# Optimization experiments

Measured on AMD Instinct MI355X. Metric: run time of the kernel, lower is better.

Reference implementation:

```python
import jax, jax.numpy as jnp
import numpy as np

S, V, E, H = 4096, 10000, 128, 256
NE, TK, NH, HD, FF, NL = 4, 2, 4, 64, 2048, 2
EPS = 1e-5
SCALE = 1.0 / np.sqrt(HD).astype(np.float32)


def setup_inputs() -> dict:
    key = jax.random.key(0)
    ks = iter(jax.random.split(key, 64))
    n = lambda shape: jax.random.normal(next(ks), shape, jnp.float32) * 0.02
    inp = {"x": jax.random.randint(next(ks), (S,), 0, V)}
    inp["emb"] = n((V, E))
    for i, din in enumerate([E, H, H]):
        inp[f"moe{i}_gw"] = n((NE, din))
        inp[f"moe{i}_gb"] = jnp.zeros((NE,), jnp.float32)
        inp[f"moe{i}_ew"] = n((NE, H, din))
        inp[f"moe{i}_eb"] = jnp.zeros((NE, H), jnp.float32)
    inp["attn_in_w"] = n((NL, 3 * H, H)); inp["attn_in_b"] = jnp.zeros((NL, 3 * H), jnp.float32)
    inp["attn_out_w"] = n((NL, H, H));    inp["attn_out_b"] = jnp.zeros((NL, H), jnp.float32)
    inp["ln1_g"] = jnp.ones((NL, H), jnp.float32); inp["ln1_b"] = jnp.zeros((NL, H), jnp.float32)
    inp["ln2_g"] = jnp.ones((NL, H), jnp.float32); inp["ln2_b"] = jnp.zeros((NL, H), jnp.float32)
    inp["ff1_w"] = n((NL, FF, H)); inp["ff1_b"] = jnp.zeros((NL, FF), jnp.float32)
    inp["ff2_w"] = n((NL, H, FF)); inp["ff2_b"] = jnp.zeros((NL, H), jnp.float32)
    inp["fc_w"] = n((H, H)); inp["fc_b"] = jnp.zeros((H,), jnp.float32)
    inp["out_w"] = n((V, H)); inp["out_b"] = jnp.zeros((V,), jnp.float32)
    return inp


def _ln(x, g, b):
    m = x.mean(-1, keepdims=True)
    v = ((x - m) ** 2).mean(-1, keepdims=True)
    return (x - m) * jax.lax.rsqrt(v + EPS) * g + b


def _moe(x, gw, gb, ew, eb):
    # x: [S, din]. Faithful quirk: experts are the top-k of TOKEN 0's gates,
    # applied to every token, weighted by each token's own top-k gate scores.
    scores = jax.nn.softmax(x @ gw.T + gb, axis=-1)            # [S, NE]
    vals, idx = jax.lax.top_k(scores, TK)                      # [S, TK]
    sel = idx[0]                                               # [TK]
    outs = jnp.einsum('si,khi->skh', x, ew[sel]) + eb[sel][None]  # [S, TK, H]
    return (outs * vals[:, :, None]).sum(axis=1)               # [S, H]


def reference(x, emb,
              moe0_gw, moe0_gb, moe0_ew, moe0_eb,
              moe1_gw, moe1_gb, moe1_ew, moe1_eb,
              moe2_gw, moe2_gb, moe2_ew, moe2_eb,
              attn_in_w, attn_in_b, attn_out_w, attn_out_b,
              ln1_g, ln1_b, ln2_g, ln2_b,
              ff1_w, ff1_b, ff2_w, ff2_b,
              fc_w, fc_b, out_w, out_b):
    h = emb[x]                                                 # [S, E]
    for gw, gb, ew, eb in [(moe0_gw, moe0_gb, moe0_ew, moe0_eb),
                           (moe1_gw, moe1_gb, moe1_ew, moe1_eb),
                           (moe2_gw, moe2_gb, moe2_ew, moe2_eb)]:
        h = _moe(h, gw, gb, ew, eb)                            # [S, H]
    for l in range(NL):  # post-norm TransformerEncoderLayer (relu, no dropout at eval)
        qkv = h @ attn_in_w[l].T + attn_in_b[l]                # [S, 3H]
        q, k, v = [t.reshape(S, NH, HD) for t in jnp.split(qkv, 3, axis=-1)]
        att = jax.nn.softmax(jnp.einsum('shd,thd->hst', q, k) * SCALE, axis=-1)
        a = jnp.einsum('hst,thd->shd', att, v).reshape(S, H)
        h = _ln(h + a @ attn_out_w[l].T + attn_out_b[l], ln1_g[l], ln1_b[l])
        ffh = jax.nn.relu(h @ ff1_w[l].T + ff1_b[l]) @ ff2_w[l].T + ff2_b[l]
        h = _ln(h + ffh, ln2_g[l], ln2_b[l])
    h = h @ fc_w.T + fc_b                                      # [S, H]
    logits = h @ out_w.T + out_b                               # [S, V]
    return jax.nn.log_softmax(logits, axis=-1)
```

## Files before the change

kernel.cpp:

```cpp
#include <hip/hip_runtime.h>
#include <math.h>

#define S_ 4096
#define V_ 10000
#define E_ 128
#define H_ 256
#define NE_ 4
#define NH_ 4
#define HD_ 64
#define FF_ 2048
#define NL_ 2
#define EPS_ 1e-5f
#define SCALE_ 0.125f
#define SPLITS_ 4

typedef __attribute__((ext_vector_type(8))) short bf16x8;
typedef __attribute__((ext_vector_type(4))) float f32x4;

static __device__ __forceinline__ short f2bf(float f) {
  unsigned u = __builtin_bit_cast(unsigned, f);
  unsigned r = (u + 0x7fffu + ((u >> 16) & 1u)) >> 16;
  return (short)r;
}
static __device__ __forceinline__ float bf2f(short s) {
  unsigned u = ((unsigned)(unsigned short)s) << 16;
  return __builtin_bit_cast(float, u);
}

struct CvtArgs {
  const float* src[9];
  short* dst[9];
  int pfx[10];
};
__global__ __launch_bounds__(256) void k_cvt(CvtArgs a) {
  int b = blockIdx.x, s = 0;
  while (b >= a.pfx[s + 1]) ++s;
  size_t base = (size_t)(b - a.pfx[s]) * 2048 + threadIdx.x * 8;
  const float* sp = a.src[s] + base;
  short* dp = a.dst[s] + base;
  float4 v0 = *(const float4*)sp;
  float4 v1 = *(const float4*)(sp + 4);
  short4 o0, o1;
  o0.x = f2bf(v0.x); o0.y = f2bf(v0.y); o0.z = f2bf(v0.z); o0.w = f2bf(v0.w);
  o1.x = f2bf(v1.x); o1.y = f2bf(v1.y); o1.z = f2bf(v1.z); o1.w = f2bf(v1.w);
  *(short4*)dp = o0;
  *(short4*)(dp + 4) = o1;
}

__global__ __launch_bounds__(256) void k_embed(const int* __restrict__ x,
                                               const float* __restrict__ emb,
                                               short* __restrict__ h) {
  int i4 = (blockIdx.x * 256 + threadIdx.x) * 4;
  int s = i4 >> 7, e = i4 & 127;
  float4 v = *(const float4*)&emb[(size_t)x[s] * E_ + e];
  short4 o;
  o.x = f2bf(v.x); o.y = f2bf(v.y); o.z = f2bf(v.z); o.w = f2bf(v.w);
  *(short4*)&h[i4] = o;
}

__global__ __launch_bounds__(256) void k_gates(const short* __restrict__ X, int din,
                                               const float* __restrict__ gw,
                                               const float* __restrict__ gb,
                                               float* __restrict__ vals,
                                               int* __restrict__ sel) {
  int wave = threadIdx.x >> 6, lane = threadIdx.x & 63;
  int s = blockIdx.x * 4 + wave;
  const short* xs = X + (size_t)s * din;
  float a0 = 0.f, a1 = 0.f, a2 = 0.f, a3 = 0.f;
  for (int i = lane; i < din; i += 64) {
    float xv = bf2f(xs[i]);
    a0 += xv * gw[0 * din + i];
    a1 += xv * gw[1 * din + i];
    a2 += xv * gw[2 * din + i];
    a3 += xv * gw[3 * din + i];
  }
#pragma unroll
  for (int off = 32; off > 0; off >>= 1) {
    a0 += __shfl_xor(a0, off, 64);
    a1 += __shfl_xor(a1, off, 64);
    a2 += __shfl_xor(a2, off, 64);
    a3 += __shfl_xor(a3, off, 64);
  }
  if (lane == 0) {
    float sc[4] = {a0 + gb[0], a1 + gb[1], a2 + gb[2], a3 + gb[3]};
    float mx = fmaxf(fmaxf(sc[0], sc[1]), fmaxf(sc[2], sc[3]));
    float sum = 0.f;
#pragma unroll
    for (int e = 0; e < 4; ++e) { sc[e] = expf(sc[e] - mx); sum += sc[e]; }
    float inv = 1.0f / sum;
#pragma unroll
    for (int e = 0; e < 4; ++e) sc[e] *= inv;
    int i0 = 0; float v0 = sc[0];
#pragma unroll
    for (int e = 1; e < 4; ++e) if (sc[e] > v0) { v0 = sc[e]; i0 = e; }
    float v1 = -1.0f; int i1 = 0;
#pragma unroll
    for (int e = 0; e < 4; ++e) if (e != i0 && sc[e] > v1) { v1 = sc[e]; i1 = e; }
    vals[2 * s + 0] = v0;
    vals[2 * s + 1] = v1;
    if (s == 0) { sel[0] = i0; sel[1] = i1; }
  }
}

template <int ACT>
__global__ __launch_bounds__(256) void k_gemm64(const short* __restrict__ A,
                                                const short* __restrict__ W,
                                                const float* __restrict__ bias,
                                                short* __restrict__ C,
                                                int M, int N, int K) {
  __shared__ short As[64][40];
  __shared__ short Bs[64][40];
  int bm = blockIdx.y * 64, bn = blockIdx.x * 64;
  int tid = threadIdx.x, lane = tid & 63, wv = tid >> 6;
  int quad = lane >> 4, m16 = lane & 15;
  int wr = (wv >> 1) * 32, wc = (wv & 1) * 32;
  int srow = tid >> 2, sc = (tid & 3) * 8;
  const short* Ar = A + (size_t)(bm + srow) * K + sc;
  const short* Wr = W + (size_t)(bn + srow) * K + sc;
  f32x4 acc[2][2];
#pragma unroll
  for (int m = 0; m < 2; ++m)
#pragma unroll
    for (int n = 0; n < 2; ++n) acc[m][n] = (f32x4){0.f, 0.f, 0.f, 0.f};
  for (int k0 = 0; k0 < K; k0 += 32) {
    *(bf16x8*)&As[srow][sc] = *(const bf16x8*)&Ar[k0];
    *(bf16x8*)&Bs[srow][sc] = *(const bf16x8*)&Wr[k0];
    __syncthreads();
    bf16x8 af[2], bf[2];
#pragma unroll
    for (int m = 0; m < 2; ++m) af[m] = *(const bf16x8*)&As[wr + m * 16 + m16][quad * 8];
#pragma unroll
    for (int n = 0; n < 2; ++n) bf[n] = *(const bf16x8*)&Bs[wc + n * 16 + m16][quad * 8];
#pragma unroll
    for (int m = 0; m < 2; ++m)
#pragma unroll
      for (int n = 0; n < 2; ++n)
        acc[m][n] = __builtin_amdgcn_mfma_f32_16x16x32_bf16(af[m], bf[n], acc[m][n], 0, 0, 0);
    __syncthreads();
  }
#pragma unroll
  for (int n = 0; n < 2; ++n) {
    int col = bn + wc + n * 16 + m16;
    float b = bias[col];
#pragma unroll
    for (int m = 0; m < 2; ++m) {
      int row0 = bm + wr + m * 16 + quad * 4;
#pragma unroll
      for (int r = 0; r < 4; ++r) {
        float v = acc[m][n][r] + b;
        if (ACT) v = fmaxf(v, 0.f);
        C[(size_t)(row0 + r) * N + col] = f2bf(v);
      }
    }
  }
}

__global__ __launch_bounds__(256) void k_moe(const short* __restrict__ A,
                                             const short* __restrict__ EW,
                                             const float* __restrict__ EB,
                                             const float* __restrict__ vals,
                                             const int* __restrict__ sel,
                                             short* __restrict__ C,
                                             int N, int K) {
  __shared__ short As[64][40];
  __shared__ short B0s[64][40];
  __shared__ short B1s[64][40];
  int e0 = sel[0], e1 = sel[1];
  const short* W0 = EW + (size_t)e0 * N * K;
  const short* W1 = EW + (size_t)e1 * N * K;
  const float* b0 = EB + (size_t)e0 * N;
  const float* b1 = EB + (size_t)e1 * N;
  int bm = blockIdx.y * 64, bn = blockIdx.x * 64;
  int tid = threadIdx.x, lane = tid & 63, wv = tid >> 6;
  int quad = lane >> 4, m16 = lane & 15;
  int wr = (wv >> 1) * 32, wc = (wv & 1) * 32;
  int srow = tid >> 2, sc = (tid & 3) * 8;
  const short* Ar = A + (size_t)(bm + srow) * K + sc;
  const short* W0r = W0 + (size_t)(bn + srow) * K + sc;
  const short* W1r = W1 + (size_t)(bn + srow) * K + sc;
  f32x4 a0[2][2], a1[2][2];
#pragma unroll
  for (int m = 0; m < 2; ++m)
#pragma unroll
    for (int n = 0; n < 2; ++n) {
      a0[m][n] = (f32x4){0.f, 0.f, 0.f, 0.f};
      a1[m][n] = (f32x4){0.f, 0.f, 0.f, 0.f};
    }
  for (int k0 = 0; k0 < K; k0 += 32) {
    *(bf16x8*)&As[srow][sc] = *(const bf16x8*)&Ar[k0];
    *(bf16x8*)&B0s[srow][sc] = *(const bf16x8*)&W0r[k0];
    *(bf16x8*)&B1s[srow][sc] = *(const bf16x8*)&W1r[k0];
    __syncthreads();
    bf16x8 af[2], bf0[2], bf1[2];
#pragma unroll
    for (int m = 0; m < 2; ++m) af[m] = *(const bf16x8*)&As[wr + m * 16 + m16][quad * 8];
#pragma unroll
    for (int n = 0; n < 2; ++n) {
      bf0[n] = *(const bf16x8*)&B0s[wc + n * 16 + m16][quad * 8];
      bf1[n] = *(const bf16x8*)&B1s[wc + n * 16 + m16][quad * 8];
    }
#pragma unroll
    for (int m = 0; m < 2; ++m)
#pragma unroll
      for (int n = 0; n < 2; ++n) {
        a0[m][n] = __builtin_amdgcn_mfma_f32_16x16x32_bf16(af[m], bf0[n], a0[m][n], 0, 0, 0);
        a1[m][n] = __builtin_amdgcn_mfma_f32_16x16x32_bf16(af[m], bf1[n], a1[m][n], 0, 0, 0);
      }
    __syncthreads();
  }
#pragma unroll
  for (int n = 0; n < 2; ++n) {
    int col = bn + wc + n * 16 + m16;
    float bb0 = b0[col], bb1 = b1[col];
#pragma unroll
    for (int m = 0; m < 2; ++m) {
      int row0 = bm + wr + m * 16 + quad * 4;
#pragma unroll
      for (int r = 0; r < 4; ++r) {
        int row = row0 + r;
        float v = vals[2 * row] * (a0[m][n][r] + bb0) + vals[2 * row + 1] * (a1[m][n][r] + bb1);
        C[(size_t)row * N + col] = f2bf(v);
      }
    }
  }
}

template <int ACT, int F32OUT>
__global__ __launch_bounds__(256) void k_gemm128(const short* __restrict__ A,
                                                 const short* __restrict__ W,
                                                 const float* __restrict__ bias,
                                                 void* __restrict__ Cv,
                                                 int M, int N, int K) {
  __shared__ short As[128][40];
  __shared__ short Bs[128][40];
  int bm = blockIdx.y * 128, bn = blockIdx.x * 128;
  int tid = threadIdx.x, lane = tid & 63, wv = tid >> 6;
  int quad = lane >> 4, m16 = lane & 15;
  int wr = (wv >> 1) * 64, wc = (wv & 1) * 64;
  int srow = tid >> 1, sc = (tid & 1) * 16;
  const short* Ar = A + (size_t)(bm + srow) * K + sc;
  int br = bn + srow;
  const short* Wr = W + (size_t)(br < N ? br : N - 1) * K + sc;
  f32x4 acc[4][4];
#pragma unroll
  for (int m = 0; m < 4; ++m)
#pragma unroll
    for (int n = 0; n < 4; ++n) acc[m][n] = (f32x4){0.f, 0.f, 0.f, 0.f};
  for (int k0 = 0; k0 < K; k0 += 32) {
    *(bf16x8*)&As[srow][sc] = *(const bf16x8*)&Ar[k0];
    *(bf16x8*)&As[srow][sc + 8] = *(const bf16x8*)&Ar[k0 + 8];
    *(bf16x8*)&Bs[srow][sc] = *(const bf16x8*)&Wr[k0];
    *(bf16x8*)&Bs[srow][sc + 8] = *(const bf16x8*)&Wr[k0 + 8];
    __syncthreads();
    bf16x8 af[4], bf[4];
#pragma unroll
    for (int m = 0; m < 4; ++m) af[m] = *(const bf16x8*)&As[wr + m * 16 + m16][quad * 8];
#pragma unroll
    for (int n = 0; n < 4; ++n) bf[n] = *(const bf16x8*)&Bs[wc + n * 16 + m16][quad * 8];
#pragma unroll
    for (int m = 0; m < 4; ++m)
#pragma unroll
      for (int n = 0; n < 4; ++n)
        acc[m][n] = __builtin_amdgcn_mfma_f32_16x16x32_bf16(af[m], bf[n], acc[m][n], 0, 0, 0);
    __syncthreads();
  }
#pragma unroll
  for (int n = 0; n < 4; ++n) {
    int col = bn + wc + n * 16 + m16;
    if (col >= N) continue;
    float b = bias[col];
#pragma unroll
    for (int m = 0; m < 4; ++m) {
      int row0 = bm + wr + m * 16 + quad * 4;
#pragma unroll
      for (int r = 0; r < 4; ++r) {
        float v = acc[m][n][r] + b;
        if (ACT) v = fmaxf(v, 0.f);
        if (F32OUT)
          ((float*)Cv)[(size_t)(row0 + r) * N + col] = v;
        else
          ((short*)Cv)[(size_t)(row0 + r) * N + col] = f2bf(v);
      }
    }
  }
}

__global__ __launch_bounds__(256) void k_attn(const short* __restrict__ qkv,
                                              float* __restrict__ Opart,
                                              float* __restrict__ Lpart) {
  __shared__ short Ks[64][72];
  __shared__ short Vt[64][72];
  __shared__ short Ps[4][16][88];
  int tid = threadIdx.x, lane = tid & 63, wv = tid >> 6;
  int quad = lane >> 4, m16 = lane & 15;
  int head = blockIdx.y, hd0 = head * HD_;
  int split = blockIdx.z;
  int qbase = blockIdx.x * 64 + wv * 16;
  bf16x8 qf[2];
  {
    const short* qr = qkv + (size_t)(qbase + m16) * (3 * H_) + hd0 + quad * 8;
    qf[0] = *(const bf16x8*)&qr[0];
    qf[1] = *(const bf16x8*)&qr[32];
  }
  f32x4 o[4];
#pragma unroll
  for (int dt = 0; dt < 4; ++dt) o[dt] = (f32x4){0.f, 0.f, 0.f, 0.f};
  float l[4] = {0.f, 0.f, 0.f, 0.f};

  int kb_end = (split + 1) * (S_ / 64 / SPLITS_);
  for (int kb = split * (S_ / 64 / SPLITS_); kb < kb_end; ++kb) {
    __syncthreads();
    {
      int key = tid >> 2, d0 = (tid & 3) * 16;
      const short* kr = qkv + (size_t)(kb * 64 + key) * (3 * H_) + H_ + hd0 + d0;
      *(bf16x8*)&Ks[key][d0] = *(const bf16x8*)&kr[0];
      *(bf16x8*)&Ks[key][d0 + 8] = *(const bf16x8*)&kr[8];
    }
    {
      int key0 = (tid & 15) * 4, d0 = (tid >> 4) * 4;
      const short* vbase = qkv + (size_t)(kb * 64 + key0) * (3 * H_) + 2 * H_ + hd0 + d0;
      short4 v0 = *(const short4*)&vbase[0];
      short4 v1 = *(const short4*)&vbase[3 * H_];
      short4 v2 = *(const short4*)&vbase[6 * H_];
      short4 v3 = *(const short4*)&vbase[9 * H_];
      short4 t0 = {v0.x, v1.x, v2.x, v3.x};
      short4 t1 = {v0.y, v1.y, v2.y, v3.y};
      short4 t2 = {v0.z, v1.z, v2.z, v3.z};
      short4 t3 = {v0.w, v1.w, v2.w, v3.w};
      *(short4*)&Vt[d0 + 0][key0] = t0;
      *(short4*)&Vt[d0 + 1][key0] = t1;
      *(short4*)&Vt[d0 + 2][key0] = t2;
      *(short4*)&Vt[d0 + 3][key0] = t3;
    }
    __syncthreads();
    f32x4 s4[4];
#pragma unroll
    for (int kt = 0; kt < 4; ++kt) {
      bf16x8 bk0 = *(const bf16x8*)&Ks[kt * 16 + m16][quad * 8];
      bf16x8 bk1 = *(const bf16x8*)&Ks[kt * 16 + m16][32 + quad * 8];
      f32x4 z = (f32x4){0.f, 0.f, 0.f, 0.f};
      z = __builtin_amdgcn_mfma_f32_16x16x32_bf16(qf[0], bk0, z, 0, 0, 0);
      z = __builtin_amdgcn_mfma_f32_16x16x32_bf16(qf[1], bk1, z, 0, 0, 0);
      s4[kt] = z;
    }
    f32x4 rs = (f32x4){0.f, 0.f, 0.f, 0.f};
#pragma unroll
    for (int kt = 0; kt < 4; ++kt) {
#pragma unroll
      for (int r = 0; r < 4; ++r) {
        float p = __expf(s4[kt][r] * SCALE_);
        rs[r] += p;
        Ps[wv][quad * 4 + r][kt * 16 + m16] = f2bf(p);
      }
    }
#pragma unroll
    for (int mask = 1; mask < 16; mask <<= 1) {
      rs[0] += __shfl_xor(rs[0], mask, 16);
      rs[1] += __shfl_xor(rs[1], mask, 16);
      rs[2] += __shfl_xor(rs[2], mask, 16);
      rs[3] += __shfl_xor(rs[3], mask, 16);
    }
#pragma unroll
    for (int r = 0; r < 4; ++r) l[r] += rs[r];
#pragma unroll
    for (int c = 0; c < 2; ++c) {
      bf16x8 pa = *(const bf16x8*)&Ps[wv][m16][c * 32 + quad * 8];
#pragma unroll
      for (int dt = 0; dt < 4; ++dt) {
        bf16x8 bv = *(const bf16x8*)&Vt[dt * 16 + m16][c * 32 + quad * 8];
        o[dt] = __builtin_amdgcn_mfma_f32_16x16x32_bf16(pa, bv, o[dt], 0, 0, 0);
      }
    }
  }
  float* Op = Opart + ((size_t)(split * NH_ + head) * S_) * 64;
#pragma unroll
  for (int dt = 0; dt < 4; ++dt) {
#pragma unroll
    for (int r = 0; r < 4; ++r) {
      int row = qbase + quad * 4 + r;
      Op[(size_t)row * 64 + dt * 16 + m16] = o[dt][r];
    }
  }
  if (m16 == 0) {
    float* Lp = Lpart + (size_t)(split * NH_ + head) * S_;
#pragma unroll
    for (int r = 0; r < 4; ++r) Lp[qbase + quad * 4 + r] = l[r];
  }
}

__global__ __launch_bounds__(256) void k_att_combine(const float* __restrict__ Opart,
                                                     const float* __restrict__ Lpart,
                                                     short* __restrict__ abuf) {
  int idx = blockIdx.x * 256 + threadIdx.x;
  int s = idx >> 8, hd = idx & 255;
  int head = hd >> 6, d = hd & 63;
  float num = 0.f, den = 0.f;
#pragma unroll
  for (int sp = 0; sp < SPLITS_; ++sp) {
    num += Opart[((size_t)(sp * NH_ + head) * S_ + s) * 64 + d];
    den += Lpart[(size_t)(sp * NH_ + head) * S_ + s];
  }
  abuf[idx] = f2bf(num / den);
}

__global__ __launch_bounds__(256) void k_add_ln(short* __restrict__ h,
                                                const short* __restrict__ t,
                                                const float* __restrict__ g,
                                                const float* __restrict__ b) {
  __shared__ float rbuf[256];
  int s = blockIdx.x, i = threadIdx.x;
  size_t off = (size_t)s * H_ + i;
  float x = bf2f(h[off]) + bf2f(t[off]);
  rbuf[i] = x;
  __syncthreads();
#pragma unroll
  for (int o = 128; o > 0; o >>= 1) {
    if (i < o) rbuf[i] += rbuf[i + o];
    __syncthreads();
  }
  float mean = rbuf[0] * (1.0f / H_);
  __syncthreads();
  float d = x - mean;
  rbuf[i] = d * d;
  __syncthreads();
#pragma unroll
  for (int o = 128; o > 0; o >>= 1) {
    if (i < o) rbuf[i] += rbuf[i + o];
    __syncthreads();
  }
  float var = rbuf[0] * (1.0f / H_);
  h[off] = f2bf(d * rsqrtf(var + EPS_) * g[i] + b[i]);
}

__global__ __launch_bounds__(256) void k_logsoftmax(float* __restrict__ out) {
  __shared__ float rbuf[256];
  int s = blockIdx.x, t = threadIdx.x;
  float* row = out + (size_t)s * V_;
  float m = -1e30f;
  for (int i = t; i < V_; i += 256) m = fmaxf(m, row[i]);
  rbuf[t] = m;
  __syncthreads();
#pragma unroll
  for (int o = 128; o > 0; o >>= 1) {
    if (t < o) rbuf[t] = fmaxf(rbuf[t], rbuf[t + o]);
    __syncthreads();
  }
  m = rbuf[0];
  __syncthreads();
  float sum = 0.f;
  for (int i = t; i < V_; i += 256) sum += expf(row[i] - m);
  rbuf[t] = sum;
  __syncthreads();
#pragma unroll
  for (int o = 128; o > 0; o >>= 1) {
    if (t < o) rbuf[t] += rbuf[t + o];
    __syncthreads();
  }
  float lse = m + logf(rbuf[0]);
  for (int i = t; i < V_; i += 256) row[i] -= lse;
}

extern "C" void kernel_launch(void* const* d_in, const int* in_sizes, int n_in,
                              void* d_out, int out_size, void* d_ws, size_t ws_size,
                              hipStream_t stream) {
  const int* x = (const int*)d_in[0];
  const float* emb = (const float*)d_in[1];
  const float* moe_gw[3] = {(const float*)d_in[2], (const float*)d_in[6], (const float*)d_in[10]};
  const float* moe_gb[3] = {(const float*)d_in[3], (const float*)d_in[7], (const float*)d_in[11]};
  const float* moe_eb[3] = {(const float*)d_in[5], (const float*)d_in[9], (const float*)d_in[13]};
  const float* attn_in_b = (const float*)d_in[15];
  const float* attn_out_b = (const float*)d_in[17];
  const float* ln1_g = (const float*)d_in[18];
  const float* ln1_b = (const float*)d_in[19];
  const float* ln2_g = (const float*)d_in[20];
  const float* ln2_b = (const float*)d_in[21];
  const float* ff1_b = (const float*)d_in[23];
  const float* ff2_b = (const float*)d_in[25];
  const float* fc_b = (const float*)d_in[27];
  const float* out_b = (const float*)d_in[29];
  float* out = (float*)d_out;

  short* wsS = (short*)d_ws;
  size_t off = 0;
  auto alloc = [&](size_t n) { short* p = wsS + off; off += n; return p; };
  short* ewb0 = alloc(131072);
  short* ewb1 = alloc(262144);
  short* ewb2 = alloc(262144);
  short* aiwb = alloc(393216);
  short* aowb = alloc(131072);
  short* f1wb = alloc(1048576);
  short* f2wb = alloc(1048576);
  short* fcwb = alloc(65536);
  short* owb  = alloc(2560000);
  short* hb_e = alloc((size_t)S_ * E_);
  short* hb_a = alloc((size_t)S_ * H_);
  short* hb_b = alloc((size_t)S_ * H_);
  short* qkvb = alloc((size_t)S_ * 3 * H_);
  short* abufb = alloc((size_t)S_ * H_);
  short* tmpb = alloc((size_t)S_ * H_);
  short* ffhb = alloc((size_t)S_ * FF_);
  float* vals = (float*)(wsS + off); off += 2 * (size_t)S_ * 2;
  int* sel = (int*)(wsS + off);
  float* Opart = (float*)ffhb;
  float* Lpart = (float*)tmpb;

  const short* moe_ewb[3] = {ewb0, ewb1, ewb2};

  CvtArgs ca;
  ca.src[0] = (const float*)d_in[4];  ca.dst[0] = ewb0;
  ca.src[1] = (const float*)d_in[8];  ca.dst[1] = ewb1;
  ca.src[2] = (const float*)d_in[12]; ca.dst[2] = ewb2;
  ca.src[3] = (const float*)d_in[14]; ca.dst[3] = aiwb;
  ca.src[4] = (const float*)d_in[16]; ca.dst[4] = aowb;
  ca.src[5] = (const float*)d_in[22]; ca.dst[5] = f1wb;
  ca.src[6] = (const float*)d_in[24]; ca.dst[6] = f2wb;
  ca.src[7] = (const float*)d_in[26]; ca.dst[7] = fcwb;
  ca.src[8] = (const float*)d_in[28]; ca.dst[8] = owb;
  int sizes[9] = {131072, 262144, 262144, 393216, 131072, 1048576, 1048576, 65536, 2560000};
  ca.pfx[0] = 0;
  for (int i = 0; i < 9; ++i) ca.pfx[i + 1] = ca.pfx[i] + sizes[i] / 2048;
  k_cvt<<<dim3(ca.pfx[9]), dim3(256), 0, stream>>>(ca);

  k_embed<<<dim3(S_ * E_ / 1024), dim3(256), 0, stream>>>(x, emb, hb_e);

  const short* moe_in[3] = {hb_e, hb_a, hb_b};
  short* moe_out[3] = {hb_a, hb_b, hb_a};
  int moe_k[3] = {E_, H_, H_};
  for (int i = 0; i < 3; ++i) {
    k_gates<<<dim3(S_ / 4), dim3(256), 0, stream>>>(moe_in[i], moe_k[i], moe_gw[i], moe_gb[i], vals, sel);
    k_moe<<<dim3(H_ / 64, S_ / 64), dim3(256), 0, stream>>>(moe_in[i], moe_ewb[i], moe_eb[i],
                                                            vals, sel, moe_out[i], H_, moe_k[i]);
  }

  for (int l = 0; l < NL_; ++l) {
    k_gemm64<0><<<dim3(3 * H_ / 64, S_ / 64), dim3(256), 0, stream>>>(
        hb_a, aiwb + (size_t)l * 3 * H_ * H_, attn_in_b + (size_t)l * 3 * H_, qkvb, S_, 3 * H_, H_);
    k_attn<<<dim3(S_ / 64, NH_, SPLITS_), dim3(256), 0, stream>>>(qkvb, Opart, Lpart);
    k_att_combine<<<dim3(S_ * H_ / 256), dim3(256), 0, stream>>>(Opart, Lpart, abufb);
    k_gemm64<0><<<dim3(H_ / 64, S_ / 64), dim3(256), 0, stream>>>(
        abufb, aowb + (size_t)l * H_ * H_, attn_out_b + (size_t)l * H_, tmpb, S_, H_, H_);
    k_add_ln<<<dim3(S_), dim3(256), 0, stream>>>(hb_a, tmpb, ln1_g + l * H_, ln1_b + l * H_);
    k_gemm128<1, 0><<<dim3(FF_ / 128, S_ / 128), dim3(256), 0, stream>>>(
        hb_a, f1wb + (size_t)l * FF_ * H_, ff1_b + (size_t)l * FF_, ffhb, S_, FF_, H_);
    k_gemm64<0><<<dim3(H_ / 64, S_ / 64), dim3(256), 0, stream>>>(
        ffhb, f2wb + (size_t)l * H_ * FF_, ff2_b + (size_t)l * H_, tmpb, S_, H_, FF_);
    k_add_ln<<<dim3(S_), dim3(256), 0, stream>>>(hb_a, tmpb, ln2_g + l * H_, ln2_b + l * H_);
  }

  k_gemm64<0><<<dim3(H_ / 64, S_ / 64), dim3(256), 0, stream>>>(hb_a, fcwb, fc_b, tmpb, S_, H_, H_);
  k_gemm128<0, 1><<<dim3((V_ + 127) / 128, S_ / 128), dim3(256), 0, stream>>>(
      tmpb, owb, out_b, out, S_, V_, H_);
  k_logsoftmax<<<dim3(S_), dim3(256), 0, stream>>>(out);
}
```

Before: 665.6 us.

## Fuse logsoftmax sums into logits GEMM, shrink tiles, warp-level layernorm

The vocab GEMM epilogue computes per-row exp partial sums into a scratch buffer, so log-softmax becomes a single subtract pass instead of three passes over the logits. N=256 GEMMs and MoE use 32-row tiles to raise block count. LayerNorm processes one row per wavefront with shuffle reductions. The fused softmax omits max subtraction, which risks overflow for large logits, and reuses the ff1 weight buffer as scratch.

```diff
diff --git a/kernel.cpp b/kernel.cpp
--- a/kernel.cpp
+++ b/kernel.cpp
@@ -13,6 +13,7 @@
 #define EPS_ 1e-5f
 #define SCALE_ 0.125f
 #define SPLITS_ 4
+#define PSTRIDE_ 160
 
 typedef __attribute__((ext_vector_type(8))) short bf16x8;
 typedef __attribute__((ext_vector_type(4))) float f32x4;
@@ -155,6 +156,49 @@
   }
 }
 
+template <int ACT>
+__global__ __launch_bounds__(256) void k_gemm32(const short* __restrict__ A,
+                                                const short* __restrict__ W,
+                                                const float* __restrict__ bias,
+                                                short* __restrict__ C,
+                                                int M, int N, int K) {
+  __shared__ short As[32][40];
+  __shared__ short Bs[64][40];
+  int bm = blockIdx.y * 32, bn = blockIdx.x * 64;
+  int tid = threadIdx.x, lane = tid & 63, wv = tid >> 6;
+  int quad = lane >> 4, m16 = lane & 15;
+  int wr = (wv >> 1) * 16, wc = (wv & 1) * 32;
+  int srow = tid >> 2, sc = (tid & 3) * 8;
+  const short* Ar = A + (size_t)(bm + (srow & 31)) * K + sc;
+  const short* Wr = W + (size_t)(bn + srow) * K + sc;
+  f32x4 acc[2];
+  acc[0] = (f32x4){0.f, 0.f, 0.f, 0.f};
+  acc[1] = (f32x4){0.f, 0.f, 0.f, 0.f};
+  for (int k0 = 0; k0 < K; k0 += 32) {
+    if (tid < 128) *(bf16x8*)&As[srow][sc] = *(const bf16x8*)&Ar[k0];
+    *(bf16x8*)&Bs[srow][sc] = *(const bf16x8*)&Wr[k0];
+    __syncthreads();
+    bf16x8 af = *(const bf16x8*)&As[wr + m16][quad * 8];
+    bf16x8 bf0 = *(const bf16x8*)&Bs[wc + m16][quad * 8];
+    bf16x8 bf1 = *(const bf16x8*)&Bs[wc + 16 + m16][quad * 8];
+    acc[0] = __builtin_amdgcn_mfma_f32_16x16x32_bf16(af, bf0, acc[0], 0, 0, 0);
+    acc[1] = __builtin_amdgcn_mfma_f32_16x16x32_bf16(af, bf1, acc[1], 0, 0, 0);
+    __syncthreads();
+  }
+#pragma unroll
+  for (int n = 0; n < 2; ++n) {
+    int col = bn + wc + n * 16 + m16;
+    float b = bias[col];
+    int row0 = bm + wr + quad * 4;
+#pragma unroll
+    for (int r = 0; r < 4; ++r) {
+      float v = acc[n][r] + b;
+      if (ACT) v = fmaxf(v, 0.f);
+      C[(size_t)(row0 + r) * N + col] = f2bf(v);
+    }
+  }
+}
+
 __global__ __launch_bounds__(256) void k_moe(const short* __restrict__ A,
                                              const short* __restrict__ EW,
                                              const float* __restrict__ EB,
@@ -162,7 +206,7 @@
                                              const int* __restrict__ sel,
                                              short* __restrict__ C,
                                              int N, int K) {
-  __shared__ short As[64][40];
+  __shared__ short As[32][40];
   __shared__ short B0s[64][40];
   __shared__ short B1s[64][40];
   int e0 = sel[0], e1 = sel[1];
@@ -170,66 +214,106 @@
   const short* W1 = EW + (size_t)e1 * N * K;
   const float* b0 = EB + (size_t)e0 * N;
   const float* b1 = EB + (size_t)e1 * N;
-  int bm = blockIdx.y * 64, bn = blockIdx.x * 64;
+  int bm = blockIdx.y * 32, bn = blockIdx.x * 64;
   int tid = threadIdx.x, lane = tid & 63, wv = tid >> 6;
   int quad = lane >> 4, m16 = lane & 15;
-  int wr = (wv >> 1) * 32, wc = (wv & 1) * 32;
+  int wr = (wv >> 1) * 16, wc = (wv & 1) * 32;
   int srow = tid >> 2, sc = (tid & 3) * 8;
-  const short* Ar = A + (size_t)(bm + srow) * K + sc;
+  const short* Ar = A + (size_t)(bm + (srow & 31)) * K + sc;
   const short* W0r = W0 + (size_t)(bn + srow) * K + sc;
   const short* W1r = W1 + (size_t)(bn + srow) * K + sc;
-  f32x4 a0[2][2], a1[2][2];
-#pragma unroll
-  for (int m = 0; m < 2; ++m)
-#pragma unroll
-    for (int n = 0; n < 2; ++n) {
-      a0[m][n] = (f32x4){0.f, 0.f, 0.f, 0.f};
-      a1[m][n] = (f32x4){0.f, 0.f, 0.f, 0.f};
-    }
+  f32x4 a0[2], a1[2];
+  a0[0] = a0[1] = (f32x4){0.f, 0.f, 0.f, 0.f};
+  a1[0] = a1[1] = (f32x4){0.f, 0.f, 0.f, 0.f};
   for (int k0 = 0; k0 < K; k0 += 32) {
-    *(bf16x8*)&As[srow][sc] = *(const bf16x8*)&Ar[k0];
+    if (tid < 128) *(bf16x8*)&As[srow][sc] = *(const bf16x8*)&Ar[k0];
     *(bf16x8*)&B0s[srow][sc] = *(const bf16x8*)&W0r[k0];
     *(bf16x8*)&B1s[srow][sc] = *(const bf16x8*)&W1r[k0];
     __syncthreads();
-    bf16x8 af[2], bf0[2], bf1[2];
-#pragma unroll
-    for (int m = 0; m < 2; ++m) af[m] = *(const bf16x8*)&As[wr + m * 16 + m16][quad * 8];
+    bf16x8 af = *(const bf16x8*)&As[wr + m16][quad * 8];
 #pragma unroll
     for (int n = 0; n < 2; ++n) {
-      bf0[n] = *(const bf16x8*)&B0s[wc + n * 16 + m16][quad * 8];
-      bf1[n] = *(const bf16x8*)&B1s[wc + n * 16 + m16][quad * 8];
-    }
-#pragma unroll
-    for (int m = 0; m < 2; ++m)
-#pragma unroll
-      for (int n = 0; n < 2; ++n) {
-        a0[m][n] = __builtin_amdgcn_mfma_f32_16x16x32_bf16(af[m], bf0[n], a0[m][n], 0, 0, 0);
-        a1[m][n] = __builtin_amdgcn_mfma_f32_16x16x32_bf16(af[m], bf1[n], a1[m][n], 0, 0, 0);
-      }
+      bf16x8 bf0 = *(const bf16x8*)&B0s[wc + n * 16 + m16][quad * 8];
+      bf16x8 bf1 = *(const bf16x8*)&B1s[wc + n * 16 + m16][quad * 8];
+      a0[n] = __builtin_amdgcn_mfma_f32_16x16x32_bf16(af, bf0, a0[n], 0, 0, 0);
+      a1[n] = __builtin_amdgcn_mfma_f32_16x16x32_bf16(af, bf1, a1[n], 0, 0, 0);
+    }
     __syncthreads();
   }
 #pragma unroll
   for (int n = 0; n < 2; ++n) {
     int col = bn + wc + n * 16 + m16;
     float bb0 = b0[col], bb1 = b1[col];
-#pragma unroll
-    for (int m = 0; m < 2; ++m) {
-      int row0 = bm + wr + m * 16 + quad * 4;
-#pragma unroll
-      for (int r = 0; r < 4; ++r) {
-        int row = row0 + r;
-        float v = vals[2 * row] * (a0[m][n][r] + bb0) + vals[2 * row + 1] * (a1[m][n][r] + bb1);
-        C[(size_t)row * N + col] = f2bf(v);
-      }
-    }
-  }
-}
-
-template <int ACT, int F32OUT>
+    int row0 = bm + wr + quad * 4;
+#pragma unroll
+    for (int r = 0; r < 4; ++r) {
+      int row = row0 + r;
+      float v = vals[2 * row] * (a0[n][r] + bb0) + vals[2 * row + 1] * (a1[n][r] + bb1);
+      C[(size_t)row * N + col] = f2bf(v);
+    }
+  }
+}
+
+template <int ACT>
 __global__ __launch_bounds__(256) void k_gemm128(const short* __restrict__ A,
                                                  const short* __restrict__ W,
                                                  const float* __restrict__ bias,
-                                                 void* __restrict__ Cv,
+                                                 short* __restrict__ C,
+                                                 int M, int N, int K) {
+  __shared__ short As[128][40];
+  __shared__ short Bs[128][40];
+  int bm = blockIdx.y * 128, bn = blockIdx.x * 128;
+  int tid = threadIdx.x, lane = tid & 63, wv = tid >> 6;
+  int quad = lane >> 4, m16 = lane & 15;
+  int wr = (wv >> 1) * 64, wc = (wv & 1) * 64;
+  int srow = tid >> 1, sc = (tid & 1) * 16;
+  const short* Ar = A + (size_t)(bm + srow) * K + sc;
+  const short* Wr = W + (size_t)(bn + srow) * K + sc;
+  f32x4 acc[4][4];
+#pragma unroll
+  for (int m = 0; m < 4; ++m)
+#pragma unroll
+    for (int n = 0; n < 4; ++n) acc[m][n] = (f32x4){0.f, 0.f, 0.f, 0.f};
+  for (int k0 = 0; k0 < K; k0 += 32) {
+    *(bf16x8*)&As[srow][sc] = *(const bf16x8*)&Ar[k0];
+    *(bf16x8*)&As[srow][sc + 8] = *(const bf16x8*)&Ar[k0 + 8];
+    *(bf16x8*)&Bs[srow][sc] = *(const bf16x8*)&Wr[k0];
+    *(bf16x8*)&Bs[srow][sc + 8] = *(const bf16x8*)&Wr[k0 + 8];
+    __syncthreads();
+    bf16x8 af[4], bf[4];
+#pragma unroll
+    for (int m = 0; m < 4; ++m) af[m] = *(const bf16x8*)&As[wr + m * 16 + m16][quad * 8];
+#pragma unroll
+    for (int n = 0; n < 4; ++n) bf[n] = *(const bf16x8*)&Bs[wc + n * 16 + m16][quad * 8];
+#pragma unroll
+    for (int m = 0; m < 4; ++m)
+#pragma unroll
+      for (int n = 0; n < 4; ++n)
+        acc[m][n] = __builtin_amdgcn_mfma_f32_16x16x32_bf16(af[m], bf[n], acc[m][n], 0, 0, 0);
+    __syncthreads();
+  }
+#pragma unroll
+  for (int n = 0; n < 4; ++n) {
+    int col = bn + wc + n * 16 + m16;
+    float b = bias[col];
+#pragma unroll
+    for (int m = 0; m < 4; ++m) {
+      int row0 = bm + wr + m * 16 + quad * 4;
+#pragma unroll
+      for (int r = 0; r < 4; ++r) {
+        float v = acc[m][n][r] + b;
+        if (ACT) v = fmaxf(v, 0.f);
+        C[(size_t)(row0 + r) * N + col] = f2bf(v);
+      }
+    }
+  }
+}
+
+__global__ __launch_bounds__(256) void k_glogits(const short* __restrict__ A,
+                                                 const short* __restrict__ W,
+                                                 const float* __restrict__ bias,
+                                                 float* __restrict__ C,
+                                                 float* __restrict__ psums,
                                                  int M, int N, int K) {
   __shared__ short As[128][40];
   __shared__ short Bs[128][40];
@@ -264,24 +348,54 @@
         acc[m][n] = __builtin_amdgcn_mfma_f32_16x16x32_bf16(af[m], bf[n], acc[m][n], 0, 0, 0);
     __syncthreads();
   }
+  float bcol[4];
+  int cvalid[4];
 #pragma unroll
   for (int n = 0; n < 4; ++n) {
     int col = bn + wc + n * 16 + m16;
-    if (col >= N) continue;
-    float b = bias[col];
-#pragma unroll
-    for (int m = 0; m < 4; ++m) {
-      int row0 = bm + wr + m * 16 + quad * 4;
-#pragma unroll
-      for (int r = 0; r < 4; ++r) {
-        float v = acc[m][n][r] + b;
-        if (ACT) v = fmaxf(v, 0.f);
-        if (F32OUT)
-          ((float*)Cv)[(size_t)(row0 + r) * N + col] = v;
-        else
-          ((short*)Cv)[(size_t)(row0 + r) * N + col] = f2bf(v);
+    cvalid[n] = (col < N);
+    bcol[n] = cvalid[n] ? bias[col] : 0.f;
+  }
+  int pslot = blockIdx.x * 2 + (wv & 1);
+#pragma unroll
+  for (int m = 0; m < 4; ++m) {
+#pragma unroll
+    for (int r = 0; r < 4; ++r) {
+      int row = bm + wr + m * 16 + quad * 4 + r;
+      float es = 0.f;
+#pragma unroll
+      for (int n = 0; n < 4; ++n) {
+        if (cvalid[n]) {
+          float v = acc[m][n][r] + bcol[n];
+          C[(size_t)row * N + (bn + wc + n * 16 + m16)] = v;
+          es += __expf(v);
+        }
       }
-    }
+#pragma unroll
+      for (int mask = 1; mask < 16; mask <<= 1) es += __shfl_xor(es, mask, 16);
+      if (m16 == 0) psums[(size_t)row * PSTRIDE_ + pslot] = es;
+    }
+  }
+}
+
+__global__ __launch_bounds__(256) void k_lsfinal(float* __restrict__ out,
+                                                 const float* __restrict__ psums,
+                                                 int nslots) {
+  __shared__ float rbuf[256];
+  int s = blockIdx.x, t = threadIdx.x;
+  rbuf[t] = (t < nslots) ? psums[(size_t)s * PSTRIDE_ + t] : 0.f;
+  __syncthreads();
+#pragma unroll
+  for (int o = 128; o > 0; o >>= 1) {
+    if (t < o) rbuf[t] += rbuf[t + o];
+    __syncthreads();
+  }
+  float lse = logf(rbuf[0]);
+  float4* row = (float4*)(out + (size_t)s * V_);
+  for (int i = t; i < V_ / 4; i += 256) {
+    float4 o4 = row[i];
+    o4.x -= lse; o4.y -= lse; o4.z -= lse; o4.w -= lse;
+    row[i] = o4;
   }
 }
 
@@ -404,60 +518,34 @@
 }
 
 __global__ __launch_bounds__(256) void k_add_ln(short* __restrict__ h,
-                                                const short* __restrict__ t,
+                                                const short* __restrict__ t_,
                                                 const float* __restrict__ g,
                                                 const float* __restrict__ b) {
-  __shared__ float rbuf[256];
-  int s = blockIdx.x, i = threadIdx.x;
-  size_t off = (size_t)s * H_ + i;
-  float x = bf2f(h[off]) + bf2f(t[off]);
-  rbuf[i] = x;
-  __syncthreads();
-#pragma unroll
-  for (int o = 128; o > 0; o >>= 1) {
-    if (i < o) rbuf[i] += rbuf[i + o];
-    __syncthreads();
-  }
-  float mean = rbuf[0] * (1.0f / H_);
-  __syncthreads();
-  float d = x - mean;
-  rbuf[i] = d * d;
-  __syncthreads();
-#pragma unroll
-  for (int o = 128; o > 0; o >>= 1) {
-    if (i < o) rbuf[i] += rbuf[i + o];
-    __syncthreads();
-  }
-  float var = rbuf[0] * (1.0f / H_);
-  h[off] = f2bf(d * rsqrtf(var + EPS_) * g[i] + b[i]);
-}
-
-__global__ __launch_bounds__(256) void k_logsoftmax(float* __restrict__ out) {
-  __shared__ float rbuf[256];
-  int s = blockIdx.x, t = threadIdx.x;
-  float* row = out + (size_t)s * V_;
-  float m = -1e30f;
-  for (int i = t; i < V_; i += 256) m = fmaxf(m, row[i]);
-  rbuf[t] = m;
-  __syncthreads();
-#pragma unroll
-  for (int o = 128; o > 0; o >>= 1) {
-    if (t < o) rbuf[t] = fmaxf(rbuf[t], rbuf[t + o]);
-    __syncthreads();
-  }
-  m = rbuf[0];
-  __syncthreads();
-  float sum = 0.f;
-  for (int i = t; i < V_; i += 256) sum += expf(row[i] - m);
-  rbuf[t] = sum;
-  __syncthreads();
-#pragma unroll
-  for (int o = 128; o > 0; o >>= 1) {
-    if (t < o) rbuf[t] += rbuf[t + o];
-    __syncthreads();
-  }
-  float lse = m + logf(rbuf[0]);
-  for (int i = t; i < V_; i += 256) row[i] -= lse;
+  int wv = threadIdx.x >> 6, lane = threadIdx.x & 63;
+  int s = blockIdx.x * 4 + wv;
+  size_t off = (size_t)s * H_ + lane * 4;
+  short4 hv = *(const short4*)&h[off];
+  short4 tv = *(const short4*)&t_[off];
+  float x[4] = {bf2f(hv.x) + bf2f(tv.x), bf2f(hv.y) + bf2f(tv.y),
+                bf2f(hv.z) + bf2f(tv.z), bf2f(hv.w) + bf2f(tv.w)};
+  float sum = x[0] + x[1] + x[2] + x[3];
+#pragma unroll
+  for (int mask = 1; mask < 64; mask <<= 1) sum += __shfl_xor(sum, mask, 64);
+  float mean = sum * (1.0f / H_);
+  float d[4], vs = 0.f;
+#pragma unroll
+  for (int i = 0; i < 4; ++i) { d[i] = x[i] - mean; vs += d[i] * d[i]; }
+#pragma unroll
+  for (int mask = 1; mask < 64; mask <<= 1) vs += __shfl_xor(vs, mask, 64);
+  float inv = rsqrtf(vs * (1.0f / H_) + EPS_);
+  float4 gv = *(const float4*)&g[lane * 4];
+  float4 bv = *(const float4*)&b[lane * 4];
+  short4 ov;
+  ov.x = f2bf(d[0] * inv * gv.x + bv.x);
+  ov.y = f2bf(d[1] * inv * gv.y + bv.y);
+  ov.z = f2bf(d[2] * inv * gv.z + bv.z);
+  ov.w = f2bf(d[3] * inv * gv.w + bv.w);
+  *(short4*)&h[off] = ov;
 }
 
 extern "C" void kernel_launch(void* const* d_in, const int* in_sizes, int n_in,
@@ -503,6 +591,7 @@
   int* sel = (int*)(wsS + off);
   float* Opart = (float*)ffhb;
   float* Lpart = (float*)tmpb;
+  float* psums = (float*)f1wb;
 
   const short* moe_ewb[3] = {ewb0, ewb1, ewb2};
 
@@ -528,7 +617,7 @@
   int moe_k[3] = {E_, H_, H_};
   for (int i = 0; i < 3; ++i) {
     k_gates<<<dim3(S_ / 4), dim3(256), 0, stream>>>(moe_in[i], moe_k[i], moe_gw[i], moe_gb[i], vals, sel);
-    k_moe<<<dim3(H_ / 64, S_ / 64), dim3(256), 0, stream>>>(moe_in[i], moe_ewb[i], moe_eb[i],
+    k_moe<<<dim3(H_ / 64, S_ / 32), dim3(256), 0, stream>>>(moe_in[i], moe_ewb[i], moe_eb[i],
                                                             vals, sel, moe_out[i], H_, moe_k[i]);
   }
 
@@ -537,18 +626,18 @@
         hb_a, aiwb + (size_t)l * 3 * H_ * H_, attn_in_b + (size_t)l * 3 * H_, qkvb, S_, 3 * H_, H_);
     k_attn<<<dim3(S_ / 64, NH_, SPLITS_), dim3(256), 0, stream>>>(qkvb, Opart, Lpart);
     k_att_combine<<<dim3(S_ * H_ / 256), dim3(256), 0, stream>>>(Opart, Lpart, abufb);
-    k_gemm64<0><<<dim3(H_ / 64, S_ / 64), dim3(256), 0, stream>>>(
+    k_gemm32<0><<<dim3(H_ / 64, S_ / 32), dim3(256), 0, stream>>>(
         abufb, aowb + (size_t)l * H_ * H_, attn_out_b + (size_t)l * H_, tmpb, S_, H_, H_);
-    k_add_ln<<<dim3(S_), dim3(256), 0, stream>>>(hb_a, tmpb, ln1_g + l * H_, ln1_b + l * H_);
-    k_gemm128<1, 0><<<dim3(FF_ / 128, S_ / 128), dim3(256), 0, stream>>>(
+    k_add_ln<<<dim3(S_ / 4), dim3(256), 0, stream>>>(hb_a, tmpb, ln1_g + l * H_, ln1_b + l * H_);
+    k_gemm128<1><<<dim3(FF_ / 128, S_ / 128), dim3(256), 0, stream>>>(
         hb_a, f1wb + (size_t)l * FF_ * H_, ff1_b + (size_t)l * FF_, ffhb, S_, FF_, H_);
-    k_gemm64<0><<<dim3(H_ / 64, S_ / 64), dim3(256), 0, stream>>>(
+    k_gemm32<0><<<dim3(H_ / 64, S_ / 32), dim3(256), 0, stream>>>(
         ffhb, f2wb + (size_t)l * H_ * FF_, ff2_b + (size_t)l * H_, tmpb, S_, H_, FF_);
-    k_add_ln<<<dim3(S_), dim3(256), 0, stream>>>(hb_a, tmpb, ln2_g + l * H_, ln2_b + l * H_);
-  }
-
-  k_gemm64<0><<<dim3(H_ / 64, S_ / 64), dim3(256), 0, stream>>>(hb_a, fcwb, fc_b, tmpb, S_, H_, H_);
-  k_gemm128<0, 1><<<dim3((V_ + 127) / 128, S_ / 128), dim3(256), 0, stream>>>(
-      tmpb, owb, out_b, out, S_, V_, H_);
-  k_logsoftmax<<<dim3(S_), dim3(256), 0, stream>>>(out);
-}
+    k_add_ln<<<dim3(S_ / 4), dim3(256), 0, stream>>>(hb_a, tmpb, ln2_g + l * H_, ln2_b + l * H_);
+  }
+
+  k_gemm32<0><<<dim3(H_ / 64, S_ / 32), dim3(256), 0, stream>>>(hb_a, fcwb, fc_b, tmpb, S_, H_, H_);
+  int nxb = (V_ + 127) / 128;
+  k_glogits<<<dim3(nxb, S_ / 128), dim3(256), 0, stream>>>(tmpb, owb, out_b, out, psums, S_, V_, H_);
+  k_lsfinal<<<dim3(S_), dim3(256), 0, stream>>>(out, psums, nxb * 2);
+}
```

Result: faster. 639.4 us (-3.9%).
